# Kernel optimization log

Measured on AMD Instinct MI355X. Metric: run time of the kernel, lower is better.

The kernel has to match this reference:

```python
import jax, jax.numpy as jnp
import numpy as np

D_MODEL = 1024
FFN_H = 4096
N_EXPERTS = 8
TOP_K = 2
AUX_COEFF = 0.01


def setup_inputs() -> dict:
    key = jax.random.key(0)
    k_x, k_r, k_w1, k_w2 = jax.random.split(key, 4)
    x = jax.random.normal(k_x, (2, 2048, D_MODEL), dtype=jnp.float32)
    Wr = jax.random.normal(k_r, (N_EXPERTS, D_MODEL), dtype=jnp.float32) * (D_MODEL ** -0.5)
    W1 = jax.random.normal(k_w1, (N_EXPERTS, FFN_H, D_MODEL), dtype=jnp.float32) * (D_MODEL ** -0.5)
    W2 = jax.random.normal(k_w2, (N_EXPERTS, D_MODEL, FFN_H), dtype=jnp.float32) * (FFN_H ** -0.5)
    return {"x": x, "Wr": Wr, "W1": W1, "W2": W2}


def reference(x, Wr, W1, W2):
    B, T, D = x.shape
    E = Wr.shape[0]
    x_flat = x.reshape(-1, D)  # (N, D)
    # Router: softmax over experts, top-k, renormalize
    router_logits = x_flat @ Wr.T  # (N, E)
    router_probs = jax.nn.softmax(router_logits, axis=-1)
    top_k_probs, top_k_indices = jax.lax.top_k(router_probs, TOP_K)
    top_k_probs = top_k_probs / (top_k_probs.sum(-1, keepdims=True) + 1e-8)
    # Dense all-expert FFN (faithful to the vectorized dispatch)
    h = jnp.einsum('nd,ehd->neh', x_flat, W1)  # (N, E, H)
    h = jax.nn.gelu(h, approximate=False)      # torch F.gelu default = erf
    out_all = jnp.einsum('neh,edh->ned', h, W2)  # (N, E, D)
    topk_out = jnp.take_along_axis(out_all, top_k_indices[:, :, None], axis=1)  # (N, K, D)
    output = (topk_out * top_k_probs[:, :, None]).sum(1)  # (N, D)
    # Load-balance aux loss (MSE to uniform)
    tokens_per_expert = router_probs.mean(0)
    aux_loss = AUX_COEFF * jnp.mean((tokens_per_expert - 1.0 / E) ** 2)
    return output.reshape(B, T, D), aux_loss
```

## Files before the change

### kernel.cpp

```cpp
#include <hip/hip_runtime.h>
#include <cstdint>
#include <cstddef>

#define N_TOK 4096
#define DM 1024
#define FH 4096
#define NE 8
#define MT_PAD 72

typedef __attribute__((ext_vector_type(8))) short short8;
typedef __attribute__((ext_vector_type(4))) float f32x4;

#define WAITV0() asm volatile("s_waitcnt vmcnt(0)" ::: "memory")

__device__ __forceinline__ unsigned short f2bf(float f) {
  unsigned u = __float_as_uint(f);
  u += 0x7fffu + ((u >> 16) & 1u);
  return (unsigned short)(u >> 16);
}

__device__ __forceinline__ float gelu_fast(float v) {
  float e = __expf(1.5957692f * v * fmaf(0.044715f, v * v, 1.0f));
  return v - v * __builtin_amdgcn_rcpf(1.0f + e);
}

__global__ void cvt_kernel(const float* __restrict__ src, unsigned short* __restrict__ dst, int n4) {
  int stride = gridDim.x * blockDim.x;
  for (int i = blockIdx.x * blockDim.x + threadIdx.x; i < n4; i += stride) {
    float4 v = reinterpret_cast<const float4*>(src)[i];
    ushort4 o;
    o.x = f2bf(v.x); o.y = f2bf(v.y); o.z = f2bf(v.z); o.w = f2bf(v.w);
    reinterpret_cast<ushort4*>(dst)[i] = o;
  }
}

__global__ void router_kernel(const float* __restrict__ x, const float* __restrict__ Wr,
                              float* __restrict__ partials, unsigned char* __restrict__ topidx,
                              float* __restrict__ pslot, unsigned short* __restrict__ xb) {
  __shared__ float sp[NE];
  int lane = threadIdx.x & 63;
  int wv = threadIdx.x >> 6;
  int token = blockIdx.x * 4 + wv;
  if (threadIdx.x < NE) sp[threadIdx.x] = 0.f;
  __syncthreads();

  const float4* xr = (const float4*)(x + (size_t)token * DM);
  ushort4* xw = (ushort4*)(xb + (size_t)token * DM);
  float acc[NE];
#pragma unroll
  for (int e = 0; e < NE; e++) acc[e] = 0.f;
#pragma unroll
  for (int d = lane; d < DM / 4; d += 64) {
    float4 xv = xr[d];
    ushort4 o;
    o.x = f2bf(xv.x); o.y = f2bf(xv.y); o.z = f2bf(xv.z); o.w = f2bf(xv.w);
    xw[d] = o;
#pragma unroll
    for (int e = 0; e < NE; e++) {
      float4 wv4 = ((const float4*)(Wr + e * DM))[d];
      acc[e] += xv.x * wv4.x + xv.y * wv4.y + xv.z * wv4.z + xv.w * wv4.w;
    }
  }
#pragma unroll
  for (int e = 0; e < NE; e++) {
#pragma unroll
    for (int off = 32; off > 0; off >>= 1) acc[e] += __shfl_xor(acc[e], off);
  }
  if (lane == 0) {
    float m = acc[0];
#pragma unroll
    for (int e = 1; e < NE; e++) m = fmaxf(m, acc[e]);
    float p[NE];
    float s = 0.f;
#pragma unroll
    for (int e = 0; e < NE; e++) { p[e] = expf(acc[e] - m); s += p[e]; }
    float inv = 1.f / s;
#pragma unroll
    for (int e = 0; e < NE; e++) p[e] *= inv;
    int i1 = 0;
#pragma unroll
    for (int e = 1; e < NE; e++) if (p[e] > p[i1]) i1 = e;
    int i2 = (i1 == 0) ? 1 : 0;
#pragma unroll
    for (int e = 0; e < NE; e++) if (e != i1 && p[e] > p[i2]) i2 = e;
    float denom = p[i1] + p[i2] + 1e-8f;
    topidx[token] = (unsigned char)(i1 | (i2 << 4));
    pslot[2 * token]     = p[i1] / denom;
    pslot[2 * token + 1] = p[i2] / denom;
#pragma unroll
    for (int e = 0; e < NE; e++) atomicAdd(&sp[e], p[e]);
  }
  __syncthreads();
  if (threadIdx.x < NE) partials[blockIdx.x * NE + threadIdx.x] = sp[threadIdx.x];
}

__global__ void scatter_kernel(const unsigned char* __restrict__ topidx,
                               int* __restrict__ counts, int* __restrict__ lists) {
  int token = blockIdx.x * blockDim.x + threadIdx.x;
  int lane = threadIdx.x & 63;
  unsigned char packed = topidx[token];
#pragma unroll
  for (int c = 0; c < 2; c++) {
    int myexp = (c == 0) ? (packed & 15) : (packed >> 4);
    int slot = 2 * token + c;
#pragma unroll
    for (int e = 0; e < NE; e++) {
      unsigned long long mask = __ballot(myexp == e);
      int cnt = __popcll(mask);
      if (cnt) {
        int base = 0;
        if (lane == 0) base = atomicAdd(&counts[e], cnt);
        base = __shfl(base, 0);
        if (myexp == e) {
          int mypos = base + __popcll(mask & ((1ull << lane) - 1ull));
          lists[e * N_TOK + mypos] = slot;
        }
      }
    }
  }
}

__global__ void tilemap_kernel(const int* __restrict__ counts, int* __restrict__ prefix,
                               int2* __restrict__ tilemap) {
  if (threadIdx.x != 0) return;
  int off = 0, tix = 0;
  for (int e = 0; e < NE; e++) {
    prefix[e] = off;
    int c = counts[e];
    int ntile = (c + 127) >> 7;
    for (int m = 0; m < ntile; m++) { tilemap[tix].x = e; tilemap[tix].y = m; tix++; }
    off += c;
  }
  prefix[NE] = off;
  while (tix < MT_PAD) { tilemap[tix].x = -1; tilemap[tix].y = 0; tix++; }
}

__global__ void aux_kernel(const float* __restrict__ partials, int nblk,
                           float* __restrict__ aux_out) {
  __shared__ float sp[NE];
  if (threadIdx.x < NE) sp[threadIdx.x] = 0.f;
  __syncthreads();
  float s = 0.f;
  for (int i = threadIdx.x; i < nblk * NE; i += 256) s += partials[i];
  atomicAdd(&sp[threadIdx.x & 7], s);
  __syncthreads();
  if (threadIdx.x == 0) {
    float a = 0.f;
#pragma unroll
    for (int e = 0; e < NE; e++) {
      float tpe = sp[e] * (1.0f / N_TOK);
      float d = tpe - 1.0f / NE;
      a += d * d;
    }
    aux_out[0] = 0.01f * (a * (1.0f / NE));
  }
}

template <int KDIM, int NT, bool IS_GEMM1>
__global__ __launch_bounds__(256) void moe_gemm128(
    const unsigned short* __restrict__ Aglob,
    const unsigned short* __restrict__ Bglob,
    const int* __restrict__ prefix,
    const int2* __restrict__ tilemap,
    const int* __restrict__ lists,
    const float* __restrict__ pslot,
    unsigned short* __restrict__ hb,
    float* __restrict__ o2) {
  const int NWG = NT * MT_PAD;
  int wg = blockIdx.x;
  int flat = (wg & 7) * (NWG >> 3) + (wg >> 3);
  int nt = flat % NT;
  int tix = flat / NT;

  int2 tm = tilemap[tix];
  if (tm.x < 0) return;
  int e = tm.x, mt = tm.y;
  int base = prefix[e];
  int cnt  = prefix[e + 1] - base;
  const int* list = lists + e * N_TOK;
  const unsigned short* B = Bglob + (size_t)e * (size_t)(NT * 128) * KDIM;

  __shared__ unsigned short As[128 * 64];
  __shared__ unsigned short Bs[128 * 64];

  int tid = threadIdx.x, wid = tid >> 6, lane = tid & 63;
  int wr = wid >> 1, wc = wid & 1;

  int swz = (((lane & 7) ^ (lane >> 3)) << 3);
  const unsigned short* ap[4];
  const unsigned short* bp[4];
#pragma unroll
  for (int i = 0; i < 4; i++) {
    int c = i * 4 + wid;
    int r = c * 8 + (lane >> 3);
    int p = mt * 128 + r;
    int pc = p < cnt ? p : cnt - 1;
    int arow = IS_GEMM1 ? (list[pc] >> 1) : (base + pc);
    ap[i] = Aglob + (size_t)arow * KDIM + swz;
    bp[i] = B + (size_t)(nt * 128 + r) * KDIM + swz;
  }

  f32x4 acc[4][4];
#pragma unroll
  for (int m = 0; m < 4; m++)
#pragma unroll
    for (int n = 0; n < 4; n++) acc[m][n] = (f32x4){0.f, 0.f, 0.f, 0.f};

  const int T = KDIM / 64;
  for (int t = 0; t < T; ++t) {
    if (t > 0) __syncthreads();
#pragma unroll
    for (int i = 0; i < 4; i++) {
      int c = i * 4 + wid;
      __builtin_amdgcn_global_load_lds((const void*)(ap[i] + (size_t)t * 64),
                                       (void*)(&As[c * 512]), 16, 0, 0);
      __builtin_amdgcn_global_load_lds((const void*)(bp[i] + (size_t)t * 64),
                                       (void*)(&Bs[c * 512]), 16, 0, 0);
    }
    WAITV0();
    __syncthreads();
#pragma unroll
    for (int ks = 0; ks < 2; ks++) {
      short8 aF[4], bF[4];
#pragma unroll
      for (int m = 0; m < 4; m++) {
        int row = wr * 64 + m * 16 + (lane & 15);
        int cswz = (ks * 64 + ((lane >> 4) << 4)) ^ ((row & 7) << 4);
        aF[m] = *(const short8*)((const char*)As + row * 128 + cswz);
      }
#pragma unroll
      for (int n = 0; n < 4; n++) {
        int row = wc * 64 + n * 16 + (lane & 15);
        int cswz = (ks * 64 + ((lane >> 4) << 4)) ^ ((row & 7) << 4);
        bF[n] = *(const short8*)((const char*)Bs + row * 128 + cswz);
      }
      __builtin_amdgcn_s_setprio(1);
#pragma unroll
      for (int m = 0; m < 4; m++)
#pragma unroll
        for (int n = 0; n < 4; n++)
          acc[m][n] = __builtin_amdgcn_mfma_f32_16x16x32_bf16(aF[m], bF[n], acc[m][n], 0, 0, 0);
      __builtin_amdgcn_s_setprio(0);
    }
  }

  int colpart = nt * 128 + wc * 64 + (lane & 15);
#pragma unroll
  for (int m = 0; m < 4; m++) {
#pragma unroll
    for (int rr = 0; rr < 4; rr++) {
      int p = mt * 128 + wr * 64 + m * 16 + (lane >> 4) * 4 + rr;
      if (p < cnt) {
        if (IS_GEMM1) {
          size_t rowbase = (size_t)(base + p) * FH + colpart;
#pragma unroll
          for (int n = 0; n < 4; n++)
            hb[rowbase + n * 16] = f2bf(gelu_fast(acc[m][n][rr]));
        } else {
          int slot = list[p];
          float sc = pslot[slot];
          size_t rowbase = (size_t)slot * DM + colpart;
#pragma unroll
          for (int n = 0; n < 4; n++) o2[rowbase + n * 16] = sc * acc[m][n][rr];
        }
      }
    }
  }
}

__global__ void combine_kernel(const float* __restrict__ o2, float* __restrict__ out) {
  int idx = blockIdx.x * blockDim.x + threadIdx.x;
  int token = idx >> 8;
  int d4 = idx & 255;
  float4 a = ((const float4*)(o2 + (size_t)(2 * token) * DM))[d4];
  float4 b = ((const float4*)(o2 + (size_t)(2 * token + 1) * DM))[d4];
  float4 s = {a.x + b.x, a.y + b.y, a.z + b.z, a.w + b.w};
  ((float4*)(out + (size_t)token * DM))[d4] = s;
}

extern "C" void kernel_launch(void* const* d_in, const int* in_sizes, int n_in,
                              void* d_out, int out_size, void* d_ws, size_t ws_size,
                              hipStream_t stream) {
  const float* x  = (const float*)d_in[0];
  const float* Wr = (const float*)d_in[1];
  const float* W1 = (const float*)d_in[2];
  const float* W2 = (const float*)d_in[3];
  float* out = (float*)d_out;

  char* ws = (char*)d_ws;
  int*   counts   = (int*)(ws + 0);
  int*   prefix   = (int*)(ws + 64);
  unsigned char* topidx = (unsigned char*)(ws + 128);
  int2*  tilemap  = (int2*)(ws + 4352);
  float* pslot    = (float*)(ws + 8192);
  float* partials = (float*)(ws + 40960);
  int*   lists    = (int*)(ws + 73728);
  unsigned short* xb  = (unsigned short*)(ws + 204800);
  unsigned short* w1b = (unsigned short*)(ws + 204800 + 8388608);
  unsigned short* w2b = (unsigned short*)(ws + 204800 + 8388608 + 67108864);
  unsigned short* hb  = (unsigned short*)(ws + 204800 + 8388608 + 2ull * 67108864);
  float*          o2  = (float*)(ws + 204800 + 8388608 + 3ull * 67108864);
  (void)in_sizes; (void)n_in; (void)ws_size;

  hipMemsetAsync(counts, 0, 32, stream);

  cvt_kernel<<<2048, 256, 0, stream>>>(W1, w1b, NE * FH * DM / 4);
  cvt_kernel<<<2048, 256, 0, stream>>>(W2, w2b, NE * DM * FH / 4);

  router_kernel<<<N_TOK / 4, 256, 0, stream>>>(x, Wr, partials, topidx, pslot, xb);
  scatter_kernel<<<N_TOK / 256, 256, 0, stream>>>(topidx, counts, lists);
  tilemap_kernel<<<1, 64, 0, stream>>>(counts, prefix, tilemap);
  aux_kernel<<<1, 256, 0, stream>>>(partials, N_TOK / 4, out + (size_t)N_TOK * DM);

  moe_gemm128<DM, FH / 128, true><<<(FH / 128) * MT_PAD, 256, 0, stream>>>(
      xb, w1b, prefix, tilemap, lists, pslot, hb, nullptr);
  moe_gemm128<FH, DM / 128, false><<<(DM / 128) * MT_PAD, 256, 0, stream>>>(
      hb, w2b, prefix, tilemap, lists, pslot, nullptr, o2);

  combine_kernel<<<N_TOK * DM / 4 / 256, 256, 0, stream>>>(o2, out);
}
```

Measured before the change: 315.8 us.

## Fuse fp32-to-bf16 weight conversion into MoE GEMM B-tile loads

Removes the two standalone weight conversion kernels and instead has each GEMM workgroup load fp32 weight tiles into registers, pack them to bf16 with v_cvt_pk_bf16_f32, and store them to LDS. This avoids writing and rereading 128 MB of bf16 weights. In exchange, each weight tile is re-read in fp32 (twice the bytes) by every M-tile of the same expert and converted repeatedly. The B path also moves from async direct-to-LDS loads to register staging, which adds latency and VGPR pressure inside the main loop.

```diff
diff --git a/kernel.cpp b/kernel.cpp
--- a/kernel.cpp
+++ b/kernel.cpp
@@ -19,19 +19,15 @@
   return (unsigned short)(u >> 16);
 }
 
+__device__ __forceinline__ unsigned pk2bf(float lo, float hi) {
+  unsigned r;
+  asm("v_cvt_pk_bf16_f32 %0, %1, %2" : "=v"(r) : "v"(lo), "v"(hi));
+  return r;
+}
+
 __device__ __forceinline__ float gelu_fast(float v) {
   float e = __expf(1.5957692f * v * fmaf(0.044715f, v * v, 1.0f));
   return v - v * __builtin_amdgcn_rcpf(1.0f + e);
-}
-
-__global__ void cvt_kernel(const float* __restrict__ src, unsigned short* __restrict__ dst, int n4) {
-  int stride = gridDim.x * blockDim.x;
-  for (int i = blockIdx.x * blockDim.x + threadIdx.x; i < n4; i += stride) {
-    float4 v = reinterpret_cast<const float4*>(src)[i];
-    ushort4 o;
-    o.x = f2bf(v.x); o.y = f2bf(v.y); o.z = f2bf(v.z); o.w = f2bf(v.w);
-    reinterpret_cast<ushort4*>(dst)[i] = o;
-  }
 }
 
 __global__ void router_kernel(const float* __restrict__ x, const float* __restrict__ Wr,
@@ -159,7 +155,7 @@
 template <int KDIM, int NT, bool IS_GEMM1>
 __global__ __launch_bounds__(256) void moe_gemm128(
     const unsigned short* __restrict__ Aglob,
-    const unsigned short* __restrict__ Bglob,
+    const float* __restrict__ Bf,
     const int* __restrict__ prefix,
     const int2* __restrict__ tilemap,
     const int* __restrict__ lists,
@@ -178,7 +174,7 @@
   int base = prefix[e];
   int cnt  = prefix[e + 1] - base;
   const int* list = lists + e * N_TOK;
-  const unsigned short* B = Bglob + (size_t)e * (size_t)(NT * 128) * KDIM;
+  const float* B = Bf + (size_t)e * (size_t)(NT * 128) * KDIM;
 
   __shared__ unsigned short As[128 * 64];
   __shared__ unsigned short Bs[128 * 64];
@@ -188,7 +184,8 @@
 
   int swz = (((lane & 7) ^ (lane >> 3)) << 3);
   const unsigned short* ap[4];
-  const unsigned short* bp[4];
+  const float* bp[4];
+  unsigned* bdst[4];
 #pragma unroll
   for (int i = 0; i < 4; i++) {
     int c = i * 4 + wid;
@@ -198,6 +195,7 @@
     int arow = IS_GEMM1 ? (list[pc] >> 1) : (base + pc);
     ap[i] = Aglob + (size_t)arow * KDIM + swz;
     bp[i] = B + (size_t)(nt * 128 + r) * KDIM + swz;
+    bdst[i] = (unsigned*)&Bs[c * 512 + lane * 8];
   }
 
   f32x4 acc[4][4];
@@ -209,16 +207,31 @@
   const int T = KDIM / 64;
   for (int t = 0; t < T; ++t) {
     if (t > 0) __syncthreads();
+    float4 b0[4], b1[4];
+#pragma unroll
+    for (int i = 0; i < 4; i++) {
+      const float4* src = (const float4*)(bp[i] + (size_t)t * 64);
+      b0[i] = src[0];
+      b1[i] = src[1];
+    }
 #pragma unroll
     for (int i = 0; i < 4; i++) {
       int c = i * 4 + wid;
       __builtin_amdgcn_global_load_lds((const void*)(ap[i] + (size_t)t * 64),
                                        (void*)(&As[c * 512]), 16, 0, 0);
-      __builtin_amdgcn_global_load_lds((const void*)(bp[i] + (size_t)t * 64),
-                                       (void*)(&Bs[c * 512]), 16, 0, 0);
     }
     WAITV0();
+#pragma unroll
+    for (int i = 0; i < 4; i++) {
+      uint4 w;
+      w.x = pk2bf(b0[i].x, b0[i].y);
+      w.y = pk2bf(b0[i].z, b0[i].w);
+      w.z = pk2bf(b1[i].x, b1[i].y);
+      w.w = pk2bf(b1[i].z, b1[i].w);
+      *(uint4*)bdst[i] = w;
+    }
     __syncthreads();
+
 #pragma unroll
     for (int ks = 0; ks < 2; ks++) {
       short8 aF[4], bF[4];
@@ -295,17 +308,12 @@
   float* pslot    = (float*)(ws + 8192);
   float* partials = (float*)(ws + 40960);
   int*   lists    = (int*)(ws + 73728);
-  unsigned short* xb  = (unsigned short*)(ws + 204800);
-  unsigned short* w1b = (unsigned short*)(ws + 204800 + 8388608);
-  unsigned short* w2b = (unsigned short*)(ws + 204800 + 8388608 + 67108864);
-  unsigned short* hb  = (unsigned short*)(ws + 204800 + 8388608 + 2ull * 67108864);
-  float*          o2  = (float*)(ws + 204800 + 8388608 + 3ull * 67108864);
+  unsigned short* xb = (unsigned short*)(ws + 204800);
+  unsigned short* hb = (unsigned short*)(ws + 204800 + 8388608);
+  float*          o2 = (float*)(ws + 204800 + 8388608 + 67108864);
   (void)in_sizes; (void)n_in; (void)ws_size;
 
   hipMemsetAsync(counts, 0, 32, stream);
-
-  cvt_kernel<<<2048, 256, 0, stream>>>(W1, w1b, NE * FH * DM / 4);
-  cvt_kernel<<<2048, 256, 0, stream>>>(W2, w2b, NE * DM * FH / 4);
 
   router_kernel<<<N_TOK / 4, 256, 0, stream>>>(x, Wr, partials, topidx, pslot, xb);
   scatter_kernel<<<N_TOK / 256, 256, 0, stream>>>(topidx, counts, lists);
@@ -313,9 +321,9 @@
   aux_kernel<<<1, 256, 0, stream>>>(partials, N_TOK / 4, out + (size_t)N_TOK * DM);
 
   moe_gemm128<DM, FH / 128, true><<<(FH / 128) * MT_PAD, 256, 0, stream>>>(
-      xb, w1b, prefix, tilemap, lists, pslot, hb, nullptr);
+      xb, W1, prefix, tilemap, lists, pslot, hb, nullptr);
   moe_gemm128<FH, DM / 128, false><<<(DM / 128) * MT_PAD, 256, 0, stream>>>(
-      hb, w2b, prefix, tilemap, lists, pslot, nullptr, o2);
+      hb, W2, prefix, tilemap, lists, pslot, nullptr, o2);
 
   combine_kernel<<<N_TOK * DM / 4 / 256, 256, 0, stream>>>(o2, out);
 }
```

Measured after the change: 360.1 us. 14.0% more time.
